# Performance work log

Hardware: AMD Instinct MI355X
Metric: run time of the kernel (lower is better)

Reference implementation:

```python
import jax, jax.numpy as jnp
import numpy as np
import math

VOCAB = 50000; D = 512; DEPTH = 6; N = 16; DCONV = 4; R = 32; DFF = 4 * D
B = 2; L = 1024

# A = -exp(A_log) with A_log = log(arange(1..N)) repeated over D  =>  A[d,n] = -(n+1)
A_CONT = -jnp.broadcast_to(jnp.arange(1.0, N + 1, dtype=jnp.float32), (D, N))


def sinusoidal(t, dim):
    half = dim // 2
    f = jnp.exp(jnp.arange(half, dtype=jnp.float32) * (-math.log(10000.0) / (half - 1)))
    e = t.astype(jnp.float32)[:, None] * f[None, :]
    return jnp.concatenate([jnp.sin(e), jnp.cos(e)], axis=-1)


def layernorm(x, g, b, eps=1e-5):
    mu = jnp.mean(x, -1, keepdims=True)
    var = jnp.mean((x - mu) ** 2, -1, keepdims=True)
    return (x - mu) * jax.lax.rsqrt(var + eps) * g + b


def ssm(x, Win, Wconv, Wdt, bdt, Dp, Wout):
    # x: [B,L,D]
    proj = x @ Win.T  # [B,L,2D+R+2N]
    xc, z, dtu, Bp, Cp = jnp.split(proj, [D, 2 * D, 2 * D + R, 2 * D + R + N], axis=-1)
    # depthwise causal conv (left pad d_conv-1 == pad both + truncate to L)
    conv = jax.lax.conv_general_dilated(
        xc.transpose(0, 2, 1), Wconv, (1,), [(DCONV - 1, 0)],
        dimension_numbers=('NCH', 'OIH', 'NCH'), feature_group_count=D)
    u = jax.nn.silu(conv.transpose(0, 2, 1))  # [B,L,D]
    dt = jax.nn.softplus(dtu @ Wdt.T + bdt)   # [B,L,D]
    At = jnp.exp(dt[..., None] * A_CONT)      # [B,L,D,N] (ZOH)
    Bu = ((At - 1.0) / (A_CONT + 1e-10)) * Bp[:, :, None, :] * u[..., None]  # [B,L,D,N]

    def step(h, xs):
        a, bu, c = xs
        h = a * h + bu                       # [B,D,N]
        return h, jnp.einsum('bn,bdn->bd', c, h)

    h0 = jnp.zeros((x.shape[0], D, N), dtype=x.dtype)
    _, ys = jax.lax.scan(step, h0, (At.transpose(1, 0, 2, 3), Bu.transpose(1, 0, 2, 3), Cp.transpose(1, 0, 2)))
    y = ys.transpose(1, 0, 2)                # [B,L,D]
    y = (y + u * Dp) * jax.nn.silu(z)
    return y @ Wout.T


def setup_inputs():
    key = jax.random.key(0)
    ks = iter(jax.random.split(key, 32))
    nrm = lambda shape: jax.random.normal(next(ks), shape, jnp.float32) * 0.02
    inp = {
        'x_t': jax.random.randint(next(ks), (B, L), 0, VOCAB + 1),
        't': jax.random.randint(next(ks), (B,), 0, 100),
        'tok_emb': nrm((VOCAB + 1, D)),
        'tmlp_w1': nrm((4 * D, D)), 'tmlp_b1': jnp.zeros((4 * D,)),
        'tmlp_w2': nrm((D, 4 * D)), 'tmlp_b2': jnp.zeros((D,)),
        'ln1_g': jnp.ones((DEPTH, D)), 'ln1_b': jnp.zeros((DEPTH, D)),
        'in_w': nrm((DEPTH, 2 * D + R + 2 * N, D)),
        'conv_w': nrm((DEPTH, D, 1, DCONV)),
        'dt_w': nrm((DEPTH, D, R)), 'dt_b': jnp.zeros((DEPTH, D)),
        'D_p': jnp.ones((DEPTH, D)),
        'out_w': nrm((DEPTH, D, D)),
        'ln2_g': jnp.ones((DEPTH, D)), 'ln2_b': jnp.zeros((DEPTH, D)),
        'mlp_w1': nrm((DEPTH, DFF, D)), 'mlp_b1': jnp.zeros((DEPTH, DFF)),
        'mlp_w2': nrm((DEPTH, D, DFF)), 'mlp_b2': jnp.zeros((DEPTH, D)),
        'lno_g': jnp.ones((D,)), 'lno_b': jnp.zeros((D,)),
        'head_w': nrm((VOCAB, D)), 'head_b': jnp.zeros((VOCAB,)),
    }
    return inp


def reference(x_t, t, tok_emb, tmlp_w1, tmlp_b1, tmlp_w2, tmlp_b2,
              ln1_g, ln1_b, in_w, conv_w, dt_w, dt_b, D_p, out_w,
              ln2_g, ln2_b, mlp_w1, mlp_b1, mlp_w2, mlp_b2,
              lno_g, lno_b, head_w, head_b):
    te = sinusoidal(t, D)
    te = jax.nn.silu(te @ tmlp_w1.T + tmlp_b1) @ tmlp_w2.T + tmlp_b2  # [B,D]
    x = tok_emb[x_t] + te[:, None, :]                                  # [B,L,D]
    for i in range(DEPTH):
        x = x + ssm(layernorm(x, ln1_g[i], ln1_b[i]),
                    in_w[i], conv_w[i], dt_w[i], dt_b[i], D_p[i], out_w[i])
        h = layernorm(x, ln2_g[i], ln2_b[i])
        x = x + jax.nn.gelu(h @ mlp_w1[i].T + mlp_b1[i], approximate=False) @ mlp_w2[i].T + mlp_b2[i]
    x = layernorm(x, lno_g, lno_b)
    return x @ head_w.T + head_b  # [B,L,VOCAB]
```

## Files before the change

kernel.cpp:

```cpp
#include <hip/hip_runtime.h>
#include <hip/hip_bf16.h>
#include <math.h>

typedef __hip_bfloat16 bf16;
typedef short s16x8 __attribute__((ext_vector_type(8)));
typedef float f32x4 __attribute__((ext_vector_type(4)));

#define M_TOK 2048
#define DD    512
#define LSEQ  1024
#define PW    1088
#define NST   16
#define RR    32
#define DFFW  2048
#define NCH   64
#define CH    16
#define PAD   36
#define NHEAD 50000
#define NHEADP 50048

__device__ __forceinline__ float bf2f(bf16 v) { return __bfloat162float(v); }
__device__ __forceinline__ float siluf(float x) { return x / (1.f + expf(-x)); }

__device__ __forceinline__ s16x8 cvt8(const f32x4& a, const f32x4& b) {
  s16x8 r;
  r[0] = (short)__bfloat16_as_ushort(__float2bfloat16(a[0]));
  r[1] = (short)__bfloat16_as_ushort(__float2bfloat16(a[1]));
  r[2] = (short)__bfloat16_as_ushort(__float2bfloat16(a[2]));
  r[3] = (short)__bfloat16_as_ushort(__float2bfloat16(a[3]));
  r[4] = (short)__bfloat16_as_ushort(__float2bfloat16(b[0]));
  r[5] = (short)__bfloat16_as_ushort(__float2bfloat16(b[1]));
  r[6] = (short)__bfloat16_as_ushort(__float2bfloat16(b[2]));
  r[7] = (short)__bfloat16_as_ushort(__float2bfloat16(b[3]));
  return r;
}

__device__ __forceinline__ void gload16(const bf16* g, bf16* l) {
  __builtin_amdgcn_global_load_lds((const __attribute__((address_space(1))) void*)g,
                                   (__attribute__((address_space(3))) void*)l, 16, 0, 0);
}

__constant__ float c_invn[NST] = {
  -1.f/1, -1.f/2, -1.f/3, -1.f/4, -1.f/5, -1.f/6, -1.f/7, -1.f/8,
  -1.f/9, -1.f/10, -1.f/11, -1.f/12, -1.f/13, -1.f/14, -1.f/15, -1.f/16 };

__global__ __launch_bounds__(256) void k_cvt(
    const float* __restrict__ src, bf16* __restrict__ dst, int n_src, int n_dst)
{
  for (int i = (blockIdx.x * 256 + threadIdx.x) * 8; i < n_dst; i += gridDim.x * 256 * 8) {
    s16x8 v;
    if (i + 8 <= n_src) {
      f32x4 a = *(const f32x4*)(src + i), b = *(const f32x4*)(src + i + 4);
      v = cvt8(a, b);
    } else {
      v = (s16x8){0,0,0,0,0,0,0,0};
    }
    *(s16x8*)((short*)dst + i) = v;
  }
}

__global__ __launch_bounds__(256) void k_te1(
    const int* __restrict__ t, const float* __restrict__ w1, const float* __restrict__ b1,
    float* __restrict__ h1)
{
  __shared__ float semb[2][512];
  int tid = threadIdx.x;
  float t0 = (float)t[0], t1 = (float)t[1];
  {
    int k = tid;
    float f = expf((float)k * (-9.210340371976184f / 255.f));
    semb[0][k]       = sinf(t0 * f);
    semb[0][k + 256] = cosf(t0 * f);
    semb[1][k]       = sinf(t1 * f);
    semb[1][k + 256] = cosf(t1 * f);
  }
  __syncthreads();
  int wave = tid >> 6, lane = tid & 63;
  int j = blockIdx.x * 4 + wave;
  const float* wr = w1 + (size_t)j * 512;
  float s0 = 0.f, s1 = 0.f;
#pragma unroll
  for (int i = 0; i < 8; ++i) {
    int k = lane + (i << 6);
    float wv = wr[k];
    s0 += wv * semb[0][k];
    s1 += wv * semb[1][k];
  }
  for (int o = 32; o; o >>= 1) { s0 += __shfl_down(s0, o); s1 += __shfl_down(s1, o); }
  if (!lane) {
    float bv = b1[j];
    h1[j]        = siluf(s0 + bv);
    h1[2048 + j] = siluf(s1 + bv);
  }
}

__global__ __launch_bounds__(256) void k_te2(
    const float* __restrict__ h1, const float* __restrict__ w2, const float* __restrict__ b2,
    float* __restrict__ te)
{
  __shared__ float sh1[2][2048];
  int tid = threadIdx.x;
  for (int idx = tid; idx < 4096; idx += 256)
    sh1[idx >> 11][idx & 2047] = h1[idx];
  __syncthreads();
  int wave = tid >> 6, lane = tid & 63;
  int d = blockIdx.x * 4 + wave;
  const float* wr = w2 + (size_t)d * 2048;
  float s0 = 0.f, s1 = 0.f;
#pragma unroll
  for (int i = 0; i < 32; ++i) {
    int k = lane + (i << 6);
    float wv = wr[k];
    s0 += wv * sh1[0][k];
    s1 += wv * sh1[1][k];
  }
  for (int o = 32; o; o >>= 1) { s0 += __shfl_down(s0, o); s1 += __shfl_down(s1, o); }
  if (!lane) {
    float bv = b2[d];
    te[d]       = s0 + bv;
    te[512 + d] = s1 + bv;
  }
}

__global__ __launch_bounds__(256) void k_embed(
    const int* __restrict__ x_t, const float* __restrict__ tok,
    const float* __restrict__ te, float* __restrict__ x)
{
  int m = blockIdx.x;
  int b = m >> 10;
  int row = x_t[m];
  const float* src = tok + (size_t)row * DD;
  for (int d = threadIdx.x; d < DD; d += 256)
    x[(size_t)m * DD + d] = src[d] + te[b * DD + d];
}

__global__ __launch_bounds__(256) void k_layernorm(
    const float* __restrict__ x, const float* __restrict__ g, const float* __restrict__ bb,
    bf16* __restrict__ out)
{
  int m = blockIdx.x;
  const float* xr = x + (size_t)m * DD;
  float2 v = ((const float2*)xr)[threadIdx.x];
  float s = v.x + v.y, ss = v.x * v.x + v.y * v.y;
  for (int o = 32; o; o >>= 1) { s += __shfl_down(s, o); ss += __shfl_down(ss, o); }
  __shared__ float ps[4], pss[4];
  int wave = threadIdx.x >> 6, lane = threadIdx.x & 63;
  if (!lane) { ps[wave] = s; pss[wave] = ss; }
  __syncthreads();
  s = ps[0] + ps[1] + ps[2] + ps[3];
  ss = pss[0] + pss[1] + pss[2] + pss[3];
  float mu = s * (1.f / DD);
  float var = ss * (1.f / DD) - mu * mu;
  float inv = rsqrtf(var + 1e-5f);
  int d = threadIdx.x * 2;
  out[(size_t)m * DD + d]     = __float2bfloat16((v.x - mu) * inv * g[d]     + bb[d]);
  out[(size_t)m * DD + d + 1] = __float2bfloat16((v.y - mu) * inv * g[d + 1] + bb[d + 1]);
}

__global__ __launch_bounds__(256) void k_conv_dt(
    const float* __restrict__ proj, const float* __restrict__ convw,
    const float* __restrict__ dtw, const float* __restrict__ dtb,
    float* __restrict__ u, float* __restrict__ dt)
{
  int m = blockIdx.x >> 1;
  int d = ((blockIdx.x & 1) << 8) + threadIdx.x;
  int b = m >> 10, l = m & 1023;
  __shared__ float dtu[RR];
  if (threadIdx.x < RR) dtu[threadIdx.x] = proj[(size_t)m * PW + 2 * DD + threadIdx.x];
  __syncthreads();
  float c = 0.f;
#pragma unroll
  for (int j = 0; j < 4; ++j) {
    int ll = l - 3 + j;
    if (ll >= 0) c += proj[(size_t)(b * LSEQ + ll) * PW + d] * convw[d * 4 + j];
  }
  u[(size_t)m * DD + d] = siluf(c);
  float s = dtb[d];
  const float* wr = dtw + (size_t)d * RR;
#pragma unroll
  for (int r = 0; r < RR; ++r) s += dtu[r] * wr[r];
  dt[(size_t)m * DD + d] = (s > 0.f) ? (s + log1pf(expf(-s))) : log1pf(expf(s));
}

__global__ __launch_bounds__(128) void k_scan1(
    const float* __restrict__ proj, const float* __restrict__ u,
    const float* __restrict__ dt, float* __restrict__ yloc,
    float* __restrict__ Ebuf, float* __restrict__ Aprod, float* __restrict__ hend)
{
  int d = (blockIdx.x << 7) + threadIdx.x;
  int c = blockIdx.y, b = blockIdx.z;
  int m0 = b * LSEQ + c * CH;
  __shared__ float sBC[CH][32];
  for (int idx = threadIdx.x; idx < CH * 32; idx += 128)
    sBC[idx >> 5][idx & 31] = proj[(size_t)(m0 + (idx >> 5)) * PW + 2 * DD + RR + (idx & 31)];
  __syncthreads();
  float h[NST];
#pragma unroll
  for (int n = 0; n < NST; ++n) h[n] = 0.f;
  float S = 0.f;
  for (int l = 0; l < CH; ++l) {
    size_t m = (size_t)(m0 + l);
    float dtv = dt[m * DD + d];
    float uv  = u[m * DD + d];
    float e1 = expf(-dtv);
    S += dtv;
    Ebuf[m * DD + d] = expf(-S);
    float p = 1.f, acc = 0.f;
#pragma unroll
    for (int n = 0; n < NST; ++n) {
      p *= e1;
      float bu = (p - 1.f) * c_invn[n] * sBC[l][n] * uv;
      h[n] = p * h[n] + bu;
      acc += sBC[l][16 + n] * h[n];
    }
    yloc[m * DD + d] = acc;
  }
  float Ec = expf(-S);
  float p = 1.f;
  size_t base = ((size_t)(b * NCH + c) * NST) * DD + d;
#pragma unroll
  for (int n = 0; n < NST; ++n) {
    p *= Ec;
    Aprod[base + (size_t)n * DD] = p;
    hend [base + (size_t)n * DD] = h[n];
  }
}

__global__ __launch_bounds__(256) void k_scan2(
    const float* __restrict__ Aprod, const float* __restrict__ hend, float* __restrict__ h0)
{
  int idx = blockIdx.x * 256 + threadIdx.x;
  int d = idx & 511;
  int n = (idx >> 9) & 15;
  int b = idx >> 13;
  float h = 0.f;
  for (int c = 0; c < NCH; ++c) {
    size_t o = ((size_t)((b * NCH + c) * NST + n)) * DD + d;
    h0[o] = h;
    h = Aprod[o] * h + hend[o];
  }
}

__global__ __launch_bounds__(128) void k_scan3(
    const float* __restrict__ proj, const float* __restrict__ u,
    const float* __restrict__ yloc, const float* __restrict__ Ebuf,
    const float* __restrict__ h0, const float* __restrict__ Dp, bf16* __restrict__ out)
{
  int d = (blockIdx.x << 7) + threadIdx.x;
  int c = blockIdx.y, b = blockIdx.z;
  int m0 = b * LSEQ + c * CH;
  __shared__ float sC[CH][NST];
  for (int idx = threadIdx.x; idx < CH * NST; idx += 128)
    sC[idx >> 4][idx & 15] = proj[(size_t)(m0 + (idx >> 4)) * PW + 2 * DD + RR + NST + (idx & 15)];
  __syncthreads();
  float hh[NST];
  size_t base = ((size_t)(b * NCH + c) * NST) * DD + d;
#pragma unroll
  for (int n = 0; n < NST; ++n) hh[n] = h0[base + (size_t)n * DD];
  float dpv = Dp[d];
  for (int l = 0; l < CH; ++l) {
    size_t m = (size_t)(m0 + l);
    float E = Ebuf[m * DD + d];
    float p = 1.f, corr = 0.f;
#pragma unroll
    for (int n = 0; n < NST; ++n) {
      p *= E;
      corr += sC[l][n] * p * hh[n];
    }
    float y = yloc[m * DD + d] + corr;
    float z = proj[m * PW + DD + d];
    float v = (y + u[m * DD + d] * dpv) * siluf(z);
    out[m * DD + d] = __float2bfloat16(v);
  }
}

template<int ACT, bool BF16OUT, bool RES, bool BIAS>
__global__ __launch_bounds__(256) void gemm_bb128(
    const bf16* __restrict__ A, const bf16* __restrict__ B,
    const float* __restrict__ bias, const float* __restrict__ res,
    void* __restrict__ Cout, int N, int K)
{
  __shared__ bf16 sA[128 * 32];
  __shared__ bf16 sB[128 * 32];
  int flat = blockIdx.y * gridDim.x + blockIdx.x;
  int qq = (gridDim.x * gridDim.y) >> 3;
  int s = (flat & 7) * qq + (flat >> 3);
  int bm = (s % gridDim.x) * 128;
  int bn = (s / gridDim.x) * 128;
  int tid = threadIdx.x;
  int wave = tid >> 6, lane = tid & 63;
  int wm = (wave >> 1) << 6, wn = (wave & 1) << 6;
  int r = lane & 15, q = lane >> 4;
  int srow = (wave << 4) + (lane >> 2);
  int scol = (lane & 3) << 3;
  const bf16* pA = A + (size_t)(bm + srow) * K + scol;
  const bf16* pB = B + (size_t)(bn + srow) * K + scol;
  bf16* lA = sA + ((wave << 4) << 5);
  bf16* lB = sB + ((wave << 4) << 5);

  f32x4 acc[4][4];
#pragma unroll
  for (int i = 0; i < 4; ++i)
#pragma unroll
    for (int j = 0; j < 4; ++j) acc[i][j] = (f32x4){0.f, 0.f, 0.f, 0.f};

  for (int k0 = 0; k0 < K; k0 += 32) {
    gload16(pA,                  lA);
    gload16(pA + (size_t)64 * K, lA + 64 * 32);
    gload16(pB,                  lB);
    gload16(pB + (size_t)64 * K, lB + 64 * 32);
    pA += 32; pB += 32;
    __syncthreads();
    s16x8 af[4], bg[4];
#pragma unroll
    for (int i = 0; i < 4; ++i) af[i] = *(s16x8*)&sA[((wm + i * 16 + r) << 5) + (q << 3)];
#pragma unroll
    for (int j = 0; j < 4; ++j) bg[j] = *(s16x8*)&sB[((wn + j * 16 + r) << 5) + (q << 3)];
#pragma unroll
    for (int i = 0; i < 4; ++i)
#pragma unroll
      for (int j = 0; j < 4; ++j)
        acc[i][j] = __builtin_amdgcn_mfma_f32_16x16x32_bf16(af[i], bg[j], acc[i][j], 0, 0, 0);
    __syncthreads();
  }

#pragma unroll
  for (int i = 0; i < 4; ++i)
#pragma unroll
    for (int j = 0; j < 4; ++j) {
      int n = bn + wn + j * 16 + r;
      if (n >= N) continue;
#pragma unroll
      for (int e = 0; e < 4; ++e) {
        int m = bm + wm + i * 16 + (q << 2) + e;
        float v = acc[i][j][e];
        if (BIAS) v += bias[n];
        if (ACT == 1) v = 0.5f * v * (1.f + erff(v * 0.70710678118f));
        if (RES) v += res[(size_t)m * N + n];
        if (BF16OUT) ((bf16*)Cout)[(size_t)m * N + n] = __float2bfloat16(v);
        else         ((float*)Cout)[(size_t)m * N + n] = v;
      }
    }
}

template<int ACT, bool BF16OUT, bool RES, bool BIAS>
__global__ __launch_bounds__(256) void gemm_bb64(
    const bf16* __restrict__ A, const bf16* __restrict__ B,
    const float* __restrict__ bias, const float* __restrict__ res,
    void* __restrict__ Cout, int N, int K)
{
  __shared__ bf16 sA[64 * 32];
  __shared__ bf16 sB[64 * 32];
  int flat = blockIdx.y * gridDim.x + blockIdx.x;
  int qq = (gridDim.x * gridDim.y) >> 3;
  int s = (flat & 7) * qq + (flat >> 3);
  int bm = (s % gridDim.x) * 64;
  int bn = (s / gridDim.x) * 64;
  int tid = threadIdx.x;
  int wave = tid >> 6, lane = tid & 63;
  int wm = (wave >> 1) << 5, wn = (wave & 1) << 5;
  int r = lane & 15, q = lane >> 4;
  int srow = (wave << 4) + (lane >> 2);
  int scol = (lane & 3) << 3;
  const bf16* pA = A + (size_t)(bm + srow) * K + scol;
  const bf16* pB = B + (size_t)(bn + srow) * K + scol;
  bf16* lA = sA + ((wave << 4) << 5);
  bf16* lB = sB + ((wave << 4) << 5);

  f32x4 acc[2][2];
#pragma unroll
  for (int i = 0; i < 2; ++i)
#pragma unroll
    for (int j = 0; j < 2; ++j) acc[i][j] = (f32x4){0.f, 0.f, 0.f, 0.f};

  for (int k0 = 0; k0 < K; k0 += 32) {
    gload16(pA, lA);
    gload16(pB, lB);
    pA += 32; pB += 32;
    __syncthreads();
    s16x8 af[2], bg[2];
#pragma unroll
    for (int i = 0; i < 2; ++i) af[i] = *(s16x8*)&sA[((wm + i * 16 + r) << 5) + (q << 3)];
#pragma unroll
    for (int j = 0; j < 2; ++j) bg[j] = *(s16x8*)&sB[((wn + j * 16 + r) << 5) + (q << 3)];
#pragma unroll
    for (int i = 0; i < 2; ++i)
#pragma unroll
      for (int j = 0; j < 2; ++j)
        acc[i][j] = __builtin_amdgcn_mfma_f32_16x16x32_bf16(af[i], bg[j], acc[i][j], 0, 0, 0);
    __syncthreads();
  }

#pragma unroll
  for (int i = 0; i < 2; ++i)
#pragma unroll
    for (int j = 0; j < 2; ++j) {
      int n = bn + wn + j * 16 + r;
#pragma unroll
      for (int e = 0; e < 4; ++e) {
        int m = bm + wm + i * 16 + (q << 2) + e;
        float v = acc[i][j][e];
        if (BIAS) v += bias[n];
        if (ACT == 1) v = 0.5f * v * (1.f + erff(v * 0.70710678118f));
        if (RES) v += res[(size_t)m * N + n];
        if (BF16OUT) ((bf16*)Cout)[(size_t)m * N + n] = __float2bfloat16(v);
        else         ((float*)Cout)[(size_t)m * N + n] = v;
      }
    }
}

template<int ACT, bool BF16OUT, bool RES, bool BIAS, bool SWZ>
__global__ __launch_bounds__(256) void gemm_abt(
    const bf16* __restrict__ A, const float* __restrict__ B,
    const float* __restrict__ bias, const float* __restrict__ res,
    void* __restrict__ Cout, int N, int K)
{
  __shared__ bf16 sA[128][PAD];
  __shared__ bf16 sB[128][PAD];
  int bn, bm;
  if (SWZ) {
    int flat = blockIdx.y * gridDim.x + blockIdx.x;
    int q = (gridDim.x * gridDim.y) >> 3;
    int s = (flat & 7) * q + (flat >> 3);
    bm = (s % gridDim.x) * 128;
    bn = (s / gridDim.x) * 128;
  } else {
    bn = blockIdx.x * 128;
    bm = blockIdx.y * 128;
  }
  int tid = threadIdx.x;
  int wave = tid >> 6, lane = tid & 63;
  int wm = (wave >> 1) << 6, wn = (wave & 1) << 6;
  int r = lane & 15, q = lane >> 4;
  int ldr = tid >> 2;
  int ldc = (tid & 3) << 3;
  f32x4 acc[4][4];
#pragma unroll
  for (int i = 0; i < 4; ++i)
#pragma unroll
    for (int j = 0; j < 4; ++j) acc[i][j] = (f32x4){0.f, 0.f, 0.f, 0.f};
  s16x8 pa[2];
  f32x4 pb[2][2];
#define GLOAD(k0)                                                              \
  {                                                                            \
    _Pragma("unroll")                                                          \
    for (int h = 0; h < 2; ++h) {                                              \
      int row = ldr + (h << 6);                                                \
      pa[h] = *(const s16x8*)(A + (size_t)(bm + row) * K + (k0) + ldc);        \
      int nrow = bn + row;                                                     \
      if (nrow < N) {                                                          \
        const float* src = B + (size_t)nrow * K + (k0) + ldc;                  \
        pb[h][0] = *(const f32x4*)src;                                         \
        pb[h][1] = *(const f32x4*)(src + 4);                                   \
      } else {                                                                 \
        pb[h][0] = (f32x4){0.f,0.f,0.f,0.f};                                   \
        pb[h][1] = (f32x4){0.f,0.f,0.f,0.f};                                   \
      }                                                                        \
    }                                                                          \
  }
  GLOAD(0);
  for (int k0 = 0; k0 < K; k0 += 32) {
#pragma unroll
    for (int h = 0; h < 2; ++h) {
      int row = ldr + (h << 6);
      *(s16x8*)&sA[row][ldc] = pa[h];
      *(s16x8*)&sB[row][ldc] = cvt8(pb[h][0], pb[h][1]);
    }
    __syncthreads();
    if (k0 + 32 < K) GLOAD(k0 + 32);
    s16x8 af[4], bg[4];
#pragma unroll
    for (int i = 0; i < 4; ++i) af[i] = *(s16x8*)&sA[wm + i * 16 + r][q << 3];
#pragma unroll
    for (int j = 0; j < 4; ++j) bg[j] = *(s16x8*)&sB[wn + j * 16 + r][q << 3];
#pragma unroll
    for (int i = 0; i < 4; ++i)
#pragma unroll
      for (int j = 0; j < 4; ++j)
        acc[i][j] = __builtin_amdgcn_mfma_f32_16x16x32_bf16(af[i], bg[j], acc[i][j], 0, 0, 0);
    __syncthreads();
  }
#undef GLOAD
#pragma unroll
  for (int i = 0; i < 4; ++i)
#pragma unroll
    for (int j = 0; j < 4; ++j) {
      int n = bn + wn + j * 16 + r;
      if (n >= N) continue;
#pragma unroll
      for (int e = 0; e < 4; ++e) {
        int m = bm + wm + i * 16 + (q << 2) + e;
        float v = acc[i][j][e];
        if (BIAS) v += bias[n];
        if (ACT == 1) v = 0.5f * v * (1.f + erff(v * 0.70710678118f));
        if (RES) v += res[(size_t)m * N + n];
        if (BF16OUT) ((bf16*)Cout)[(size_t)m * N + n] = __float2bfloat16(v);
        else         ((float*)Cout)[(size_t)m * N + n] = v;
      }
    }
}

template<int ACT, bool BF16OUT, bool RES, bool BIAS>
__global__ __launch_bounds__(256) void gemm64(
    const bf16* __restrict__ A, const float* __restrict__ B,
    const float* __restrict__ bias, const float* __restrict__ res,
    void* __restrict__ Cout, int N, int K)
{
  __shared__ bf16 sA[64][PAD];
  __shared__ bf16 sB[64][PAD];
  int bn = blockIdx.x * 64;
  int bm = blockIdx.y * 64;
  int tid = threadIdx.x;
  int wave = tid >> 6, lane = tid & 63;
  int wm = (wave >> 1) << 5, wn = (wave & 1) << 5;
  int r = lane & 15, q = lane >> 4;
  int ldr = tid >> 2;
  int ldc = (tid & 3) << 3;
  f32x4 acc[2][2];
#pragma unroll
  for (int i = 0; i < 2; ++i)
#pragma unroll
    for (int j = 0; j < 2; ++j) acc[i][j] = (f32x4){0.f, 0.f, 0.f, 0.f};
  s16x8 pa;
  f32x4 pb[2];
#define GLOAD64(k0)                                                            \
  {                                                                            \
    pa = *(const s16x8*)(A + (size_t)(bm + ldr) * K + (k0) + ldc);             \
    const float* src = B + (size_t)(bn + ldr) * K + (k0) + ldc;                \
    pb[0] = *(const f32x4*)src;                                                \
    pb[1] = *(const f32x4*)(src + 4);                                          \
  }
  GLOAD64(0);
  for (int k0 = 0; k0 < K; k0 += 32) {
    *(s16x8*)&sA[ldr][ldc] = pa;
    *(s16x8*)&sB[ldr][ldc] = cvt8(pb[0], pb[1]);
    __syncthreads();
    if (k0 + 32 < K) GLOAD64(k0 + 32);
    s16x8 af[2], bg[2];
#pragma unroll
    for (int i = 0; i < 2; ++i) af[i] = *(s16x8*)&sA[wm + i * 16 + r][q << 3];
#pragma unroll
    for (int j = 0; j < 2; ++j) bg[j] = *(s16x8*)&sB[wn + j * 16 + r][q << 3];
#pragma unroll
    for (int i = 0; i < 2; ++i)
#pragma unroll
      for (int j = 0; j < 2; ++j)
        acc[i][j] = __builtin_amdgcn_mfma_f32_16x16x32_bf16(af[i], bg[j], acc[i][j], 0, 0, 0);
    __syncthreads();
  }
#undef GLOAD64
#pragma unroll
  for (int i = 0; i < 2; ++i)
#pragma unroll
    for (int j = 0; j < 2; ++j) {
      int n = bn + wn + j * 16 + r;
#pragma unroll
      for (int e = 0; e < 4; ++e) {
        int m = bm + wm + i * 16 + (q << 2) + e;
        float v = acc[i][j][e];
        if (BIAS) v += bias[n];
        if (ACT == 1) v = 0.5f * v * (1.f + erff(v * 0.70710678118f));
        if (RES) v += res[(size_t)m * N + n];
        if (BF16OUT) ((bf16*)Cout)[(size_t)m * N + n] = __float2bfloat16(v);
        else         ((float*)Cout)[(size_t)m * N + n] = v;
      }
    }
}

extern "C" void kernel_launch(void* const* d_in, const int* in_sizes, int n_in,
                              void* d_out, int out_size, void* d_ws, size_t ws_size,
                              hipStream_t stream) {
  const int*   x_t     = (const int*)d_in[0];
  const int*   t       = (const int*)d_in[1];
  const float* tok_emb = (const float*)d_in[2];
  const float* tmlp_w1 = (const float*)d_in[3];
  const float* tmlp_b1 = (const float*)d_in[4];
  const float* tmlp_w2 = (const float*)d_in[5];
  const float* tmlp_b2 = (const float*)d_in[6];
  const float* ln1_g   = (const float*)d_in[7];
  const float* ln1_b   = (const float*)d_in[8];
  const float* in_w    = (const float*)d_in[9];
  const float* conv_w  = (const float*)d_in[10];
  const float* dt_w    = (const float*)d_in[11];
  const float* dt_b    = (const float*)d_in[12];
  const float* D_p     = (const float*)d_in[13];
  const float* out_w   = (const float*)d_in[14];
  const float* ln2_g   = (const float*)d_in[15];
  const float* ln2_b   = (const float*)d_in[16];
  const float* mlp_w1  = (const float*)d_in[17];
  const float* mlp_b1  = (const float*)d_in[18];
  const float* mlp_w2  = (const float*)d_in[19];
  const float* mlp_b2  = (const float*)d_in[20];
  const float* lno_g   = (const float*)d_in[21];
  const float* lno_b   = (const float*)d_in[22];
  const float* head_w  = (const float*)d_in[23];
  const float* head_b  = (const float*)d_in[24];

  char* w = (char*)d_ws;
  float* te    = (float*)w;  w += 4096;
  float* h1t   = (float*)w;  w += 16384;
  float* x     = (float*)w;  w += (size_t)M_TOK * DD * 4;
  bf16*  aIn   = (bf16*)w;   w += (size_t)M_TOK * DD * 2;
  float* proj  = (float*)w;  w += (size_t)M_TOK * PW * 4;
  float* ubuf  = (float*)w;  w += (size_t)M_TOK * DD * 4;
  float* dtbuf = (float*)w;  w += (size_t)M_TOK * DD * 4;
  float* ybuf  = (float*)w;  w += (size_t)M_TOK * DD * 4;
  float* Ebuf  = (float*)w;  w += (size_t)M_TOK * DD * 4;
  float* Aprod = (float*)w;  w += (size_t)2 * NCH * NST * DD * 4;
  float* hend  = (float*)w;  w += (size_t)2 * NCH * NST * DD * 4;
  float* h0    = (float*)w;  w += (size_t)2 * NCH * NST * DD * 4;
  bf16*  gbuf  = (bf16*)proj;
  bf16* bw_in   = (bf16*)w;  w += (size_t)6 * PW * DD * 2;
  bf16* bw_out  = (bf16*)w;  w += (size_t)6 * DD * DD * 2;
  bf16* bw_m1   = (bf16*)w;  w += (size_t)6 * DFFW * DD * 2;
  bf16* bw_m2   = (bf16*)w;  w += (size_t)6 * DD * DFFW * 2;
  bf16* bw_head = (bf16*)w;  w += (size_t)NHEADP * DD * 2;
  bool fast = ((size_t)(w - (char*)d_ws) <= ws_size);

  if (fast) {
    k_cvt<<<1024, 256, 0, stream>>>(in_w,   bw_in,   6 * PW * DD,   6 * PW * DD);
    k_cvt<<<1024, 256, 0, stream>>>(out_w,  bw_out,  6 * DD * DD,   6 * DD * DD);
    k_cvt<<<1024, 256, 0, stream>>>(mlp_w1, bw_m1,   6 * DFFW * DD, 6 * DFFW * DD);
    k_cvt<<<1024, 256, 0, stream>>>(mlp_w2, bw_m2,   6 * DD * DFFW, 6 * DD * DFFW);
    k_cvt<<<2048, 256, 0, stream>>>(head_w, bw_head, NHEAD * DD,    NHEADP * DD);
  }

  k_te1<<<512, 256, 0, stream>>>(t, tmlp_w1, tmlp_b1, h1t);
  k_te2<<<128, 256, 0, stream>>>(h1t, tmlp_w2, tmlp_b2, te);
  k_embed<<<M_TOK, 256, 0, stream>>>(x_t, tok_emb, te, x);

  for (int i = 0; i < 6; ++i) {
    const float* cw_i   = conv_w + (size_t)i * DD * 4;
    const float* dtw_i  = dt_w   + (size_t)i * DD * RR;
    const float* dtb_i  = dt_b   + (size_t)i * DD;
    const float* dp_i   = D_p    + (size_t)i * DD;
    const float* m1b_i  = mlp_b1 + (size_t)i * DFFW;
    const float* m2b_i  = mlp_b2 + (size_t)i * DD;

    k_layernorm<<<M_TOK, 256, 0, stream>>>(x, ln1_g + i * DD, ln1_b + i * DD, aIn);
    if (fast)
      gemm_bb64<0,false,false,false><<<dim3(M_TOK / 64, PW / 64), 256, 0, stream>>>(
          aIn, bw_in + (size_t)i * PW * DD, nullptr, nullptr, proj, PW, DD);
    else
      gemm64<0,false,false,false><<<dim3(PW / 64, M_TOK / 64), 256, 0, stream>>>(
          aIn, in_w + (size_t)i * PW * DD, nullptr, nullptr, proj, PW, DD);
    k_conv_dt<<<M_TOK * 2, 256, 0, stream>>>(proj, cw_i, dtw_i, dtb_i, ubuf, dtbuf);
    k_scan1<<<dim3(4, NCH, 2), 128, 0, stream>>>(proj, ubuf, dtbuf, ybuf, Ebuf, Aprod, hend);
    k_scan2<<<2 * NST * DD / 256, 256, 0, stream>>>(Aprod, hend, h0);
    k_scan3<<<dim3(4, NCH, 2), 128, 0, stream>>>(proj, ubuf, ybuf, Ebuf, h0, dp_i, aIn);
    if (fast) {
      gemm_bb64<0,false,true,false><<<dim3(M_TOK / 64, DD / 64), 256, 0, stream>>>(
          aIn, bw_out + (size_t)i * DD * DD, nullptr, x, x, DD, DD);
      k_layernorm<<<M_TOK, 256, 0, stream>>>(x, ln2_g + i * DD, ln2_b + i * DD, aIn);
      gemm_bb128<1,true,false,true><<<dim3(M_TOK / 128, DFFW / 128), 256, 0, stream>>>(
          aIn, bw_m1 + (size_t)i * DFFW * DD, m1b_i, nullptr, gbuf, DFFW, DD);
      gemm_bb64<0,false,true,true><<<dim3(M_TOK / 64, DD / 64), 256, 0, stream>>>(
          gbuf, bw_m2 + (size_t)i * DD * DFFW, m2b_i, x, x, DD, DFFW);
    } else {
      gemm64<0,false,true,false><<<dim3(DD / 64, M_TOK / 64), 256, 0, stream>>>(
          aIn, out_w + (size_t)i * DD * DD, nullptr, x, x, DD, DD);
      k_layernorm<<<M_TOK, 256, 0, stream>>>(x, ln2_g + i * DD, ln2_b + i * DD, aIn);
      gemm64<1,true,false,true><<<dim3(DFFW / 64, M_TOK / 64), 256, 0, stream>>>(
          aIn, mlp_w1 + (size_t)i * DFFW * DD, m1b_i, nullptr, gbuf, DFFW, DD);
      gemm64<0,false,true,true><<<dim3(DD / 64, M_TOK / 64), 256, 0, stream>>>(
          gbuf, mlp_w2 + (size_t)i * DD * DFFW, m2b_i, x, x, DD, DFFW);
    }
  }

  k_layernorm<<<M_TOK, 256, 0, stream>>>(x, lno_g, lno_b, aIn);
  if (fast)
    gemm_bb128<0,false,false,true><<<dim3(M_TOK / 128, NHEADP / 128), 256, 0, stream>>>(
        aIn, bw_head, head_b, nullptr, d_out, NHEAD, DD);
  else
    gemm_abt<0,false,false,true,true><<<dim3(M_TOK / 128, (NHEAD + 127) / 128), 256, 0, stream>>>(
        aIn, head_w, head_b, nullptr, d_out, NHEAD, DD);
}
```

Baseline: 1.160 ms.

## Fuse conv/dt into scan pass one and double-buffer GEMM shared tiles

The depthwise conv, SiLU, dt projection and softplus are folded into the first scan kernel, which now reads conv inputs straight from proj using a sliding window. This removes one launch per layer, the dt buffer, and a write-then-read round trip for u and dt. Separately, both bf16 MFMA GEMMs now double-buffer their LDS tiles, issuing the next K-slice loads before computing on the current one and dropping one barrier per iteration. The fused scan kernel runs only 512 blocks, so the conv/dt work moves onto a low-parallelism grid, and the GEMMs use twice the shared memory.

```diff
diff --git a/kernel.cpp b/kernel.cpp
--- a/kernel.cpp
+++ b/kernel.cpp
@@ -157,51 +157,53 @@
   out[(size_t)m * DD + d + 1] = __float2bfloat16((v.y - mu) * inv * g[d + 1] + bb[d + 1]);
 }
 
-__global__ __launch_bounds__(256) void k_conv_dt(
+__global__ __launch_bounds__(128) void k_scan1f(
     const float* __restrict__ proj, const float* __restrict__ convw,
     const float* __restrict__ dtw, const float* __restrict__ dtb,
-    float* __restrict__ u, float* __restrict__ dt)
-{
-  int m = blockIdx.x >> 1;
-  int d = ((blockIdx.x & 1) << 8) + threadIdx.x;
-  int b = m >> 10, l = m & 1023;
-  __shared__ float dtu[RR];
-  if (threadIdx.x < RR) dtu[threadIdx.x] = proj[(size_t)m * PW + 2 * DD + threadIdx.x];
-  __syncthreads();
-  float c = 0.f;
-#pragma unroll
-  for (int j = 0; j < 4; ++j) {
-    int ll = l - 3 + j;
-    if (ll >= 0) c += proj[(size_t)(b * LSEQ + ll) * PW + d] * convw[d * 4 + j];
-  }
-  u[(size_t)m * DD + d] = siluf(c);
-  float s = dtb[d];
-  const float* wr = dtw + (size_t)d * RR;
-#pragma unroll
-  for (int r = 0; r < RR; ++r) s += dtu[r] * wr[r];
-  dt[(size_t)m * DD + d] = (s > 0.f) ? (s + log1pf(expf(-s))) : log1pf(expf(s));
-}
-
-__global__ __launch_bounds__(128) void k_scan1(
-    const float* __restrict__ proj, const float* __restrict__ u,
-    const float* __restrict__ dt, float* __restrict__ yloc,
+    float* __restrict__ ubuf, float* __restrict__ yloc,
     float* __restrict__ Ebuf, float* __restrict__ Aprod, float* __restrict__ hend)
 {
   int d = (blockIdx.x << 7) + threadIdx.x;
   int c = blockIdx.y, b = blockIdx.z;
   int m0 = b * LSEQ + c * CH;
   __shared__ float sBC[CH][32];
-  for (int idx = threadIdx.x; idx < CH * 32; idx += 128)
-    sBC[idx >> 5][idx & 31] = proj[(size_t)(m0 + (idx >> 5)) * PW + 2 * DD + RR + (idx & 31)];
+  __shared__ float sDT[CH][32];
+  for (int idx = threadIdx.x; idx < CH * 32; idx += 128) {
+    int l = idx >> 5, j = idx & 31;
+    sBC[l][j] = proj[(size_t)(m0 + l) * PW + 2 * DD + RR + j];
+    sDT[l][j] = proj[(size_t)(m0 + l) * PW + 2 * DD + j];
+  }
   __syncthreads();
+  float cw0 = convw[d * 4], cw1 = convw[d * 4 + 1], cw2 = convw[d * 4 + 2], cw3 = convw[d * 4 + 3];
+  float dtbd = dtb[d];
+  f32x4 wr[8];
+#pragma unroll
+  for (int i = 0; i < 8; ++i) wr[i] = *(const f32x4*)(dtw + (size_t)d * RR + i * 4);
+  float w0 = 0.f, w1 = 0.f, w2 = 0.f;
+  {
+    int l0 = c * CH;
+    if (l0 >= 3) w0 = proj[(size_t)(m0 - 3) * PW + d];
+    if (l0 >= 2) w1 = proj[(size_t)(m0 - 2) * PW + d];
+    if (l0 >= 1) w2 = proj[(size_t)(m0 - 1) * PW + d];
+  }
   float h[NST];
 #pragma unroll
   for (int n = 0; n < NST; ++n) h[n] = 0.f;
   float S = 0.f;
   for (int l = 0; l < CH; ++l) {
     size_t m = (size_t)(m0 + l);
-    float dtv = dt[m * DD + d];
-    float uv  = u[m * DD + d];
+    float xc = proj[m * PW + d];
+    float cv = w0 * cw0 + w1 * cw1 + w2 * cw2 + xc * cw3;
+    w0 = w1; w1 = w2; w2 = xc;
+    float uv = siluf(cv);
+    ubuf[m * DD + d] = uv;
+    float s = dtbd;
+#pragma unroll
+    for (int i = 0; i < 8; ++i) {
+      f32x4 q = *(const f32x4*)&sDT[l][i * 4];
+      s += q[0] * wr[i][0] + q[1] * wr[i][1] + q[2] * wr[i][2] + q[3] * wr[i][3];
+    }
+    float dtv = (s > 0.f) ? (s + log1pf(expf(-s))) : log1pf(expf(s));
     float e1 = expf(-dtv);
     S += dtv;
     Ebuf[m * DD + d] = expf(-S);
@@ -280,8 +282,8 @@
     const float* __restrict__ bias, const float* __restrict__ res,
     void* __restrict__ Cout, int N, int K)
 {
-  __shared__ bf16 sA[128 * 32];
-  __shared__ bf16 sB[128 * 32];
+  __shared__ bf16 sA[2][128 * 32];
+  __shared__ bf16 sB[2][128 * 32];
   int flat = blockIdx.y * gridDim.x + blockIdx.x;
   int qq = (gridDim.x * gridDim.y) >> 3;
   int s = (flat & 7) * qq + (flat >> 3);
@@ -295,8 +297,7 @@
   int scol = (lane & 3) << 3;
   const bf16* pA = A + (size_t)(bm + srow) * K + scol;
   const bf16* pB = B + (size_t)(bn + srow) * K + scol;
-  bf16* lA = sA + ((wave << 4) << 5);
-  bf16* lB = sB + ((wave << 4) << 5);
+  int lbase = (wave << 4) << 5;
 
   f32x4 acc[4][4];
 #pragma unroll
@@ -304,24 +305,36 @@
 #pragma unroll
     for (int j = 0; j < 4; ++j) acc[i][j] = (f32x4){0.f, 0.f, 0.f, 0.f};
 
+  gload16(pA,                  sA[0] + lbase);
+  gload16(pA + (size_t)64 * K, sA[0] + lbase + 64 * 32);
+  gload16(pB,                  sB[0] + lbase);
+  gload16(pB + (size_t)64 * K, sB[0] + lbase + 64 * 32);
+  pA += 32; pB += 32;
+  __syncthreads();
+
+  int cur = 0;
   for (int k0 = 0; k0 < K; k0 += 32) {
-    gload16(pA,                  lA);
-    gload16(pA + (size_t)64 * K, lA + 64 * 32);
-    gload16(pB,                  lB);
-    gload16(pB + (size_t)64 * K, lB + 64 * 32);
-    pA += 32; pB += 32;
-    __syncthreads();
+    if (k0 + 32 < K) {
+      gload16(pA,                  sA[cur ^ 1] + lbase);
+      gload16(pA + (size_t)64 * K, sA[cur ^ 1] + lbase + 64 * 32);
+      gload16(pB,                  sB[cur ^ 1] + lbase);
+      gload16(pB + (size_t)64 * K, sB[cur ^ 1] + lbase + 64 * 32);
+      pA += 32; pB += 32;
+    }
     s16x8 af[4], bg[4];
 #pragma unroll
-    for (int i = 0; i < 4; ++i) af[i] = *(s16x8*)&sA[((wm + i * 16 + r) << 5) + (q << 3)];
-#pragma unroll
-    for (int j = 0; j < 4; ++j) bg[j] = *(s16x8*)&sB[((wn + j * 16 + r) << 5) + (q << 3)];
+    for (int i = 0; i < 4; ++i) af[i] = *(s16x8*)&sA[cur][((wm + i * 16 + r) << 5) + (q << 3)];
+#pragma unroll
+    for (int j = 0; j < 4; ++j) bg[j] = *(s16x8*)&sB[cur][((wn + j * 16 + r) << 5) + (q << 3)];
 #pragma unroll
     for (int i = 0; i < 4; ++i)
 #pragma unroll
       for (int j = 0; j < 4; ++j)
         acc[i][j] = __builtin_amdgcn_mfma_f32_16x16x32_bf16(af[i], bg[j], acc[i][j], 0, 0, 0);
-    __syncthreads();
+    if (k0 + 32 < K) {
+      __syncthreads();
+      cur ^= 1;
+    }
   }
 
 #pragma unroll
@@ -349,8 +362,8 @@
     const float* __restrict__ bias, const float* __restrict__ res,
     void* __restrict__ Cout, int N, int K)
 {
-  __shared__ bf16 sA[64 * 32];
-  __shared__ bf16 sB[64 * 32];
+  __shared__ bf16 sA[2][64 * 32];
+  __shared__ bf16 sB[2][64 * 32];
   int flat = blockIdx.y * gridDim.x + blockIdx.x;
   int qq = (gridDim.x * gridDim.y) >> 3;
   int s = (flat & 7) * qq + (flat >> 3);
@@ -364,8 +377,7 @@
   int scol = (lane & 3) << 3;
   const bf16* pA = A + (size_t)(bm + srow) * K + scol;
   const bf16* pB = B + (size_t)(bn + srow) * K + scol;
-  bf16* lA = sA + ((wave << 4) << 5);
-  bf16* lB = sB + ((wave << 4) << 5);
+  int lbase = (wave << 4) << 5;
 
   f32x4 acc[2][2];
 #pragma unroll
@@ -373,22 +385,32 @@
 #pragma unroll
     for (int j = 0; j < 2; ++j) acc[i][j] = (f32x4){0.f, 0.f, 0.f, 0.f};
 
+  gload16(pA, sA[0] + lbase);
+  gload16(pB, sB[0] + lbase);
+  pA += 32; pB += 32;
+  __syncthreads();
+
+  int cur = 0;
   for (int k0 = 0; k0 < K; k0 += 32) {
-    gload16(pA, lA);
-    gload16(pB, lB);
-    pA += 32; pB += 32;
-    __syncthreads();
+    if (k0 + 32 < K) {
+      gload16(pA, sA[cur ^ 1] + lbase);
+      gload16(pB, sB[cur ^ 1] + lbase);
+      pA += 32; pB += 32;
+    }
     s16x8 af[2], bg[2];
 #pragma unroll
-    for (int i = 0; i < 2; ++i) af[i] = *(s16x8*)&sA[((wm + i * 16 + r) << 5) + (q << 3)];
-#pragma unroll
-    for (int j = 0; j < 2; ++j) bg[j] = *(s16x8*)&sB[((wn + j * 16 + r) << 5) + (q << 3)];
+    for (int i = 0; i < 2; ++i) af[i] = *(s16x8*)&sA[cur][((wm + i * 16 + r) << 5) + (q << 3)];
+#pragma unroll
+    for (int j = 0; j < 2; ++j) bg[j] = *(s16x8*)&sB[cur][((wn + j * 16 + r) << 5) + (q << 3)];
 #pragma unroll
     for (int i = 0; i < 2; ++i)
 #pragma unroll
       for (int j = 0; j < 2; ++j)
         acc[i][j] = __builtin_amdgcn_mfma_f32_16x16x32_bf16(af[i], bg[j], acc[i][j], 0, 0, 0);
-    __syncthreads();
+    if (k0 + 32 < K) {
+      __syncthreads();
+      cur ^= 1;
+    }
   }
 
 #pragma unroll
@@ -603,7 +625,6 @@
   bf16*  aIn   = (bf16*)w;   w += (size_t)M_TOK * DD * 2;
   float* proj  = (float*)w;  w += (size_t)M_TOK * PW * 4;
   float* ubuf  = (float*)w;  w += (size_t)M_TOK * DD * 4;
-  float* dtbuf = (float*)w;  w += (size_t)M_TOK * DD * 4;
   float* ybuf  = (float*)w;  w += (size_t)M_TOK * DD * 4;
   float* Ebuf  = (float*)w;  w += (size_t)M_TOK * DD * 4;
   float* Aprod = (float*)w;  w += (size_t)2 * NCH * NST * DD * 4;
@@ -644,8 +665,8 @@
     else
       gemm64<0,false,false,false><<<dim3(PW / 64, M_TOK / 64), 256, 0, stream>>>(
           aIn, in_w + (size_t)i * PW * DD, nullptr, nullptr, proj, PW, DD);
-    k_conv_dt<<<M_TOK * 2, 256, 0, stream>>>(proj, cw_i, dtw_i, dtb_i, ubuf, dtbuf);
-    k_scan1<<<dim3(4, NCH, 2), 128, 0, stream>>>(proj, ubuf, dtbuf, ybuf, Ebuf, Aprod, hend);
+    k_scan1f<<<dim3(4, NCH, 2), 128, 0, stream>>>(proj, cw_i, dtw_i, dtb_i,
+                                                  ubuf, ybuf, Ebuf, Aprod, hend);
     k_scan2<<<2 * NST * DD / 256, 256, 0, stream>>>(Aprod, hend, h0);
     k_scan3<<<dim3(4, NCH, 2), 128, 0, stream>>>(proj, ubuf, ybuf, Ebuf, h0, dp_i, aIn);
     if (fast) {
```

New measurement: 1.250 ms. +7.7%, slower.
